# Performance work log

Measured on AMD Instinct MI355X. Metric: run time of the kernel, lower is better.

Reference implementation:

```python
import jax, jax.numpy as jnp
import numpy as np

QD, CD, H, N, Z, R = 1280, 768, 8, 2, 2, 8
BF, S = 16, 4096


def setup_inputs() -> dict:
    key = jax.random.key(0)
    ks = jax.random.split(key, 12)
    inp = {
        "x": jax.random.normal(ks[0], (BF, S, QD), jnp.float32),
        "context": jax.random.normal(ks[1], (BF, N, CD), jnp.float32),
        "Wq": jax.random.normal(ks[2], (QD, QD), jnp.float32) * (1.0 / np.sqrt(QD)),
        "Wk": jax.random.normal(ks[3], (QD, CD), jnp.float32) * (1.0 / np.sqrt(CD)),
        "Ak": jax.random.normal(ks[4], (R, CD), jnp.float32) * 0.01,
        "Bk": jax.random.normal(ks[5], (QD, R), jnp.float32) * 0.01,
        "Wv": jax.random.normal(ks[6], (QD, CD), jnp.float32) * (1.0 / np.sqrt(CD)),
        "Av": jax.random.normal(ks[7], (R, CD), jnp.float32) * 0.01,
        "Bv": jax.random.normal(ks[8], (QD, R), jnp.float32) * 0.01,
        "depth_pe": jax.random.normal(ks[9], (Z, CD), jnp.float32) * 0.02,
        "Wout": jax.random.normal(ks[10], (QD, QD), jnp.float32) * (1.0 / np.sqrt(QD)),
        "bout": jnp.zeros((QD,), jnp.float32),
    }
    return inp


def _lora(t, W, A, B):
    # F.linear(t, W) + F.linear(F.linear(t, A), B)
    return t @ W.T + (t @ A.T) @ B.T


def reference(x, context, Wq, Wk, Ak, Bk, Wv, Av, Bv, depth_pe, Wout, bout):
    bf, s, qd = x.shape
    d = qd // H
    scale = 1.0 / jnp.sqrt(jnp.asarray(d, x.dtype))
    # expand context with depth positional encoding: [bf, N, Z, CD] -> [bf, N*Z, CD]
    ctx3d = (context[:, :, None, :] + depth_pe[None, None, :, :]).reshape(bf, N * Z, -1)
    Q = (x @ Wq.T).reshape(bf, s, H, d).transpose(0, 2, 1, 3)            # bf h s d
    K = _lora(ctx3d, Wk, Ak, Bk).reshape(bf, N * Z, H, d).transpose(0, 2, 1, 3)  # bf h t d
    V = _lora(ctx3d, Wv, Av, Bv).reshape(bf, N * Z, H, d).transpose(0, 2, 1, 3)
    scores = jnp.einsum('bhsd,bhtd->bhst', Q, K) * scale                 # bf h s (n z)
    sigma = jax.nn.sigmoid(scores).reshape(bf, H, s, N, Z)
    sigma_mean = sigma.mean(axis=1)                                      # bf s n z
    opacity = jnp.minimum(sigma_mean.sum(axis=2), 1.0)                   # bf s z
    ones = jnp.ones((bf, s, 1), x.dtype)
    T = jnp.cumprod(jnp.concatenate([ones, 1.0 - opacity], axis=-1), axis=-1)[:, :, :-1]  # bf s z
    weights = (T[:, None, :, None, :] * sigma).reshape(bf, H, s, N * Z)
    out = jnp.einsum('bhst,bhtd->bhsd', weights, V)
    out = out.transpose(0, 2, 1, 3).reshape(bf, s, qd)
    return x + out @ Wout.T + bout
```

## Files before the change

### kernel.cpp

```cpp
#include <hip/hip_runtime.h>

#define QD   1280
#define CD   768
#define NH   8
#define NN   2
#define ZZ   2
#define RR   8
#define BFB  16
#define SS   4096
#define DH   160
#define TT   4
#define OO   32

typedef __attribute__((ext_vector_type(4))) float f32x4;
typedef __attribute__((ext_vector_type(8))) short short8;

__global__ __launch_bounds__(256) void kv_kernel(
    const float* __restrict__ ctx, const float* __restrict__ pe,
    const float* __restrict__ Wk, const float* __restrict__ Ak, const float* __restrict__ Bk,
    const float* __restrict__ Wv, const float* __restrict__ Av, const float* __restrict__ Bv,
    float* __restrict__ Kf, float* __restrict__ Vf)
{
    const int jt = blockIdx.x, t = blockIdx.y, b = blockIdx.z;
    const int n = t >> 1, z = t & 1;
    const int tid = threadIdx.x;
    __shared__ float sctx[CD];
    __shared__ float sa[16];

    for (int c = tid; c < CD; c += 256)
        sctx[c] = ctx[(b * NN + n) * CD + c] + pe[z * CD + c];
    __syncthreads();

    const int wave = tid >> 6, lane = tid & 63;
    for (int q = 0; q < 4; q++) {
        const int idx = wave * 4 + q;
        const float* Arow = (idx < 8 ? Ak : Av) + (idx & 7) * CD;
        float p = 0.f;
        for (int c = lane; c < CD; c += 64) p += sctx[c] * Arow[c];
        for (int off = 32; off; off >>= 1) p += __shfl_down(p, off);
        if (lane == 0) sa[idx] = p;
    }
    __syncthreads();

    const int j = jt * 256 + tid;
    float accK = 0.f, accV = 0.f;
    {
        f32x4 bk0 = *(const f32x4*)(Bk + j * RR);
        f32x4 bk1 = *(const f32x4*)(Bk + j * RR + 4);
        f32x4 bv0 = *(const f32x4*)(Bv + j * RR);
        f32x4 bv1 = *(const f32x4*)(Bv + j * RR + 4);
#pragma unroll
        for (int r = 0; r < 4; r++) {
            accK += sa[r] * bk0[r] + sa[r + 4] * bk1[r];
            accV += sa[8 + r] * bv0[r] + sa[12 + r] * bv1[r];
        }
    }
    const f32x4* wkrow = (const f32x4*)(Wk + j * CD);
    const f32x4* wvrow = (const f32x4*)(Wv + j * CD);
    for (int c4 = 0; c4 < CD / 4; c4++) {
        f32x4 wk = wkrow[c4], wv = wvrow[c4];
#pragma unroll
        for (int u = 0; u < 4; u++) {
            float xc = sctx[c4 * 4 + u];
            accK += xc * wk[u];
            accV += xc * wv[u];
        }
    }
    Kf[(b * TT + t) * QD + j] = accK;
    Vf[(b * TT + t) * QD + j] = accV;
}

__global__ __launch_bounds__(256) void pvw_kernel(
    const float* __restrict__ Wq, const float* __restrict__ Wout,
    const float* __restrict__ Kf, const float* __restrict__ Vf,
    float* __restrict__ P, float* __restrict__ VW)
{
    const int which = blockIdx.x, ht = blockIdx.y, b = blockIdx.z;
    const int h = ht >> 2, t = ht & 3;
    const int tid = threadIdx.x;
    __shared__ float sv[DH];

    if (which == 0) {
        for (int d = tid; d < DH; d += 256) sv[d] = Kf[(b * TT + t) * QD + h * DH + d];
        __syncthreads();
        float acc[5] = {0.f, 0.f, 0.f, 0.f, 0.f};
        for (int d = 0; d < DH; d++) {
            float kd = sv[d];
            const float* wqrow = Wq + (h * DH + d) * QD;
#pragma unroll
            for (int i = 0; i < 5; i++) acc[i] += kd * wqrow[tid + 256 * i];
        }
#pragma unroll
        for (int i = 0; i < 5; i++)
            P[(b * QD + tid + 256 * i) * OO + ht] = acc[i];
    } else {
        for (int d = tid; d < DH; d += 256) sv[d] = Vf[(b * TT + t) * QD + h * DH + d];
        __syncthreads();
        float acc[5] = {0.f, 0.f, 0.f, 0.f, 0.f};
        for (int d4 = 0; d4 < DH / 4; d4++) {
#pragma unroll
            for (int i = 0; i < 5; i++) {
                int j = tid + 256 * i;
                f32x4 w = *(const f32x4*)(Wout + j * QD + h * DH + d4 * 4);
#pragma unroll
                for (int u = 0; u < 4; u++) acc[i] += sv[d4 * 4 + u] * w[u];
            }
        }
#pragma unroll
        for (int i = 0; i < 5; i++)
            VW[(b * OO + ht) * QD + tid + 256 * i] = acc[i];
    }
}

__global__ __launch_bounds__(64) void pfrag_kernel(
    const float* __restrict__ P, unsigned* __restrict__ Pfrag)
{
    const int ksnt = blockIdx.x;
    const int b = blockIdx.y;
    const int ks = ksnt >> 1, nt = ksnt & 1;
    const int l = threadIdx.x;
    const int k0 = ks * 32 + (l >> 4) * 8;
    const int o  = nt * 16 + (l & 15);

    const float* Pb = P + ((size_t)b * QD + k0) * OO + o;
    float v[8];
#pragma unroll
    for (int j = 0; j < 8; j++) v[j] = Pb[j * OO];

    unsigned d[4];
#pragma unroll
    for (int i = 0; i < 4; i++)
        asm("v_cvt_pk_bf16_f32 %0, %1, %2" : "=v"(d[i]) : "v"(v[2 * i]), "v"(v[2 * i + 1]));

    unsigned* dst = Pfrag + ((size_t)(b * 80 + ksnt) * 64 + l) * 4;
    dst[0] = d[0]; dst[1] = d[1]; dst[2] = d[2]; dst[3] = d[3];
}

__global__ __launch_bounds__(256) void scores_kernel(
    const float* __restrict__ x, const unsigned* __restrict__ Pfrag,
    float* __restrict__ Wgt)
{
    const int b = blockIdx.y;
    const int tid = threadIdx.x;
    const int w = tid >> 6, l = tid & 63;
    const int lg = l >> 4, lo16 = l & 15;
    const int rowbase = blockIdx.x * 64 + w * 16;
    const float scale = 0.07905694150420949f;

    f32x4 acc0 = (f32x4){0.f, 0.f, 0.f, 0.f};
    f32x4 acc1 = (f32x4){0.f, 0.f, 0.f, 0.f};

    const float* xr0 = x + ((size_t)b * SS + rowbase + lo16) * QD;
    const unsigned* Pfb = Pfrag + (size_t)b * 80 * 256 + (size_t)l * 4;

    union U { unsigned u[4]; short8 s; };

    for (int ks = 0; ks < 40; ++ks) {
        const int kb = ks * 32 + lg * 8;
        f32x4 x00 = *(const f32x4*)(xr0 + kb);
        f32x4 x01 = *(const f32x4*)(xr0 + kb + 4);
        short8 bf0 = *(const short8*)(Pfb + (size_t)(ks * 2 + 0) * 256);
        short8 bf1 = *(const short8*)(Pfb + (size_t)(ks * 2 + 1) * 256);

        U a0;
        asm("v_cvt_pk_bf16_f32 %0, %1, %2" : "=v"(a0.u[0]) : "v"(x00[0]), "v"(x00[1]));
        asm("v_cvt_pk_bf16_f32 %0, %1, %2" : "=v"(a0.u[1]) : "v"(x00[2]), "v"(x00[3]));
        asm("v_cvt_pk_bf16_f32 %0, %1, %2" : "=v"(a0.u[2]) : "v"(x01[0]), "v"(x01[1]));
        asm("v_cvt_pk_bf16_f32 %0, %1, %2" : "=v"(a0.u[3]) : "v"(x01[2]), "v"(x01[3]));

        acc0 = __builtin_amdgcn_mfma_f32_16x16x32_bf16(a0.s, bf0, acc0, 0, 0, 0);
        acc1 = __builtin_amdgcn_mfma_f32_16x16x32_bf16(a0.s, bf1, acc1, 0, 0, 0);
    }

#pragma unroll
    for (int r = 0; r < 4; ++r) {
        float s0v = 1.f / (1.f + __expf(-acc0[r] * scale));
        float s1v = 1.f / (1.f + __expf(-acc1[r] * scale));
        float contrib = ((l & 1) == 0) ? (s0v + s1v) : 0.f;
        contrib += __shfl_xor(contrib, 1);
        contrib += __shfl_xor(contrib, 2);
        contrib += __shfl_xor(contrib, 4);
        contrib += __shfl_xor(contrib, 8);
        float op0 = fminf(contrib * 0.125f, 1.f);
        float t1 = (l & 1) ? (1.f - op0) : 1.f;
        const int R = rowbase + lg * 4 + r;
        float* Wr = Wgt + ((size_t)b * SS + R) * OO;
        Wr[lo16]      = s0v * t1;
        Wr[lo16 + 16] = s1v * t1;
    }
}

__global__ __launch_bounds__(320) void out_kernel(
    const float* __restrict__ x, const float* __restrict__ bout,
    const float* __restrict__ VW, const float* __restrict__ Wgt,
    float* __restrict__ out)
{
    const int b = blockIdx.y;
    const int s0 = blockIdx.x * 64;
    const int tid = threadIdx.x;

    f32x4 vw[32];
    {
        const float* VWb = VW + (size_t)b * OO * QD + 4 * tid;
#pragma unroll
        for (int ht = 0; ht < 32; ht++) vw[ht] = *(const f32x4*)(VWb + ht * QD);
    }
    f32x4 bo = *(const f32x4*)(bout + 4 * tid);

    const size_t base = ((size_t)b * SS + s0) * QD + 4 * tid;
    const float* wg0 = Wgt + ((size_t)b * SS + s0) * OO;

#pragma unroll 2
    for (int row = 0; row < 64; ++row) {
        f32x4 acc = bo + *(const f32x4*)(x + base + (size_t)row * QD);
        const float* wr = wg0 + row * OO;
#pragma unroll
        for (int ht = 0; ht < 32; ht++) {
            float wv_ = wr[ht];
            acc += wv_ * vw[ht];
        }
        *(f32x4*)(out + base + (size_t)row * QD) = acc;
    }
}

extern "C" void kernel_launch(void* const* d_in, const int* in_sizes, int n_in,
                              void* d_out, int out_size, void* d_ws, size_t ws_size,
                              hipStream_t stream) {
    const float* x    = (const float*)d_in[0];
    const float* ctx  = (const float*)d_in[1];
    const float* Wq   = (const float*)d_in[2];
    const float* Wk   = (const float*)d_in[3];
    const float* Ak   = (const float*)d_in[4];
    const float* Bk   = (const float*)d_in[5];
    const float* Wv   = (const float*)d_in[6];
    const float* Av   = (const float*)d_in[7];
    const float* Bv   = (const float*)d_in[8];
    const float* pe   = (const float*)d_in[9];
    const float* Wout = (const float*)d_in[10];
    const float* bout = (const float*)d_in[11];
    float* out = (float*)d_out;

    float* ws = (float*)d_ws;
    float* Kf = ws;
    float* Vf = ws + 81920;
    float* P  = ws + 163840;
    float* VW = ws + 819200;
    float* Wg = ws + 1474560;
    unsigned* Pfrag = (unsigned*)(ws + 3571712);

    kv_kernel<<<dim3(5, 4, 16), 256, 0, stream>>>(ctx, pe, Wk, Ak, Bk, Wv, Av, Bv, Kf, Vf);
    pvw_kernel<<<dim3(2, 32, 16), 256, 0, stream>>>(Wq, Wout, Kf, Vf, P, VW);
    pfrag_kernel<<<dim3(80, 16), 64, 0, stream>>>(P, Pfrag);
    scores_kernel<<<dim3(64, 16), 256, 0, stream>>>(x, Pfrag, Wg);
    out_kernel<<<dim3(64, 16), 320, 0, stream>>>(x, bout, VW, Wg, out);
}
```

Before: 940.5 us.

## Share weight loads across kv slots in pvw and split-K scores kernel

The pvw kernel now computes all four context slots per head in one block. Each Wq/Wout element is loaded once and reused for four accumulators, where before each slot reloaded the weights, and the grid shrinks to a quarter. The scores kernel doubles to 512 threads and splits the K dimension across two wave groups, combining partial MFMA accumulators through shared memory. This gives more waves to hide memory latency on the x reads, at the cost of a barrier and LDS traffic.

```diff
diff --git a/kernel.cpp b/kernel.cpp
--- a/kernel.cpp
+++ b/kernel.cpp
@@ -75,40 +75,68 @@
     const float* __restrict__ Kf, const float* __restrict__ Vf,
     float* __restrict__ P, float* __restrict__ VW)
 {
-    const int which = blockIdx.x, ht = blockIdx.y, b = blockIdx.z;
-    const int h = ht >> 2, t = ht & 3;
+    const int which = blockIdx.x, h = blockIdx.y, b = blockIdx.z;
     const int tid = threadIdx.x;
-    __shared__ float sv[DH];
+    __shared__ float sv[TT][DH];
+
+    const float* src = (which == 0 ? Kf : Vf);
+    for (int e = tid; e < TT * DH; e += 256) {
+        int t = e / DH, d = e % DH;
+        sv[t][d] = src[(b * TT + t) * QD + h * DH + d];
+    }
+    __syncthreads();
 
     if (which == 0) {
-        for (int d = tid; d < DH; d += 256) sv[d] = Kf[(b * TT + t) * QD + h * DH + d];
-        __syncthreads();
-        float acc[5] = {0.f, 0.f, 0.f, 0.f, 0.f};
+        float acc[5][4];
+#pragma unroll
+        for (int i = 0; i < 5; i++)
+#pragma unroll
+            for (int t = 0; t < 4; t++) acc[i][t] = 0.f;
+
+#pragma unroll 2
         for (int d = 0; d < DH; d++) {
-            float kd = sv[d];
             const float* wqrow = Wq + (h * DH + d) * QD;
-#pragma unroll
-            for (int i = 0; i < 5; i++) acc[i] += kd * wqrow[tid + 256 * i];
-        }
+            float wq[5];
+#pragma unroll
+            for (int i = 0; i < 5; i++) wq[i] = wqrow[tid + 256 * i];
+#pragma unroll
+            for (int i = 0; i < 5; i++)
+#pragma unroll
+                for (int t = 0; t < 4; t++)
+                    acc[i][t] = fmaf(sv[t][d], wq[i], acc[i][t]);
+        }
+#pragma unroll
+        for (int i = 0; i < 5; i++) {
+            int j = tid + 256 * i;
+            f32x4 v = {acc[i][0], acc[i][1], acc[i][2], acc[i][3]};
+            *(f32x4*)(P + ((size_t)(b * QD + j)) * OO + h * 4) = v;
+        }
+    } else {
+        float acc[5][4];
 #pragma unroll
         for (int i = 0; i < 5; i++)
-            P[(b * QD + tid + 256 * i) * OO + ht] = acc[i];
-    } else {
-        for (int d = tid; d < DH; d += 256) sv[d] = Vf[(b * TT + t) * QD + h * DH + d];
-        __syncthreads();
-        float acc[5] = {0.f, 0.f, 0.f, 0.f, 0.f};
+#pragma unroll
+            for (int t = 0; t < 4; t++) acc[i][t] = 0.f;
+
         for (int d4 = 0; d4 < DH / 4; d4++) {
 #pragma unroll
             for (int i = 0; i < 5; i++) {
                 int j = tid + 256 * i;
-                f32x4 w = *(const f32x4*)(Wout + j * QD + h * DH + d4 * 4);
-#pragma unroll
-                for (int u = 0; u < 4; u++) acc[i] += sv[d4 * 4 + u] * w[u];
+                f32x4 w = *(const f32x4*)(Wout + (size_t)j * QD + h * DH + d4 * 4);
+#pragma unroll
+                for (int u = 0; u < 4; u++)
+#pragma unroll
+                    for (int t = 0; t < 4; t++)
+                        acc[i][t] = fmaf(sv[t][d4 * 4 + u], w[u], acc[i][t]);
             }
         }
 #pragma unroll
-        for (int i = 0; i < 5; i++)
-            VW[(b * OO + ht) * QD + tid + 256 * i] = acc[i];
+        for (int i = 0; i < 5; i++) {
+            int j = tid + 256 * i;
+#pragma unroll
+            for (int t = 0; t < 4; t++)
+                VW[((size_t)b * OO + h * 4 + t) * QD + j] = acc[i][t];
+        }
     }
 }
 
@@ -136,26 +164,31 @@
     dst[0] = d[0]; dst[1] = d[1]; dst[2] = d[2]; dst[3] = d[3];
 }
 
-__global__ __launch_bounds__(256) void scores_kernel(
+__global__ __launch_bounds__(512, 8) void scores_kernel(
     const float* __restrict__ x, const unsigned* __restrict__ Pfrag,
     float* __restrict__ Wgt)
 {
     const int b = blockIdx.y;
     const int tid = threadIdx.x;
     const int w = tid >> 6, l = tid & 63;
+    const int g = w & 3;
+    const int khalf = w >> 2;
     const int lg = l >> 4, lo16 = l & 15;
-    const int rowbase = blockIdx.x * 64 + w * 16;
+    const int rowbase = blockIdx.x * 64 + g * 16;
     const float scale = 0.07905694150420949f;
+
+    __shared__ float red[4][64][9];
 
     f32x4 acc0 = (f32x4){0.f, 0.f, 0.f, 0.f};
     f32x4 acc1 = (f32x4){0.f, 0.f, 0.f, 0.f};
 
-    const float* xr0 = x + ((size_t)b * SS + rowbase + lo16) * QD;
-    const unsigned* Pfb = Pfrag + (size_t)b * 80 * 256 + (size_t)l * 4;
+    const float* xr0 = x + ((size_t)b * SS + rowbase + lo16) * QD + khalf * 640;
+    const unsigned* Pfb = Pfrag + (size_t)b * 80 * 256 + (size_t)l * 4
+                        + (size_t)khalf * 40 * 256;
 
     union U { unsigned u[4]; short8 s; };
 
-    for (int ks = 0; ks < 40; ++ks) {
+    for (int ks = 0; ks < 20; ++ks) {
         const int kb = ks * 32 + lg * 8;
         f32x4 x00 = *(const f32x4*)(xr0 + kb);
         f32x4 x01 = *(const f32x4*)(xr0 + kb + 4);
@@ -170,6 +203,22 @@
 
         acc0 = __builtin_amdgcn_mfma_f32_16x16x32_bf16(a0.s, bf0, acc0, 0, 0, 0);
         acc1 = __builtin_amdgcn_mfma_f32_16x16x32_bf16(a0.s, bf1, acc1, 0, 0, 0);
+    }
+
+    if (khalf == 1) {
+#pragma unroll
+        for (int r = 0; r < 4; ++r) {
+            red[g][l][r]     = acc0[r];
+            red[g][l][4 + r] = acc1[r];
+        }
+    }
+    __syncthreads();
+    if (khalf == 1) return;
+
+#pragma unroll
+    for (int r = 0; r < 4; ++r) {
+        acc0[r] += red[g][l][r];
+        acc1[r] += red[g][l][4 + r];
     }
 
 #pragma unroll
@@ -249,8 +298,8 @@
     unsigned* Pfrag = (unsigned*)(ws + 3571712);
 
     kv_kernel<<<dim3(5, 4, 16), 256, 0, stream>>>(ctx, pe, Wk, Ak, Bk, Wv, Av, Bv, Kf, Vf);
-    pvw_kernel<<<dim3(2, 32, 16), 256, 0, stream>>>(Wq, Wout, Kf, Vf, P, VW);
+    pvw_kernel<<<dim3(2, 8, 16), 256, 0, stream>>>(Wq, Wout, Kf, Vf, P, VW);
     pfrag_kernel<<<dim3(80, 16), 64, 0, stream>>>(P, Pfrag);
-    scores_kernel<<<dim3(64, 16), 256, 0, stream>>>(x, Pfrag, Wg);
+    scores_kernel<<<dim3(64, 16), 512, 0, stream>>>(x, Pfrag, Wg);
     out_kernel<<<dim3(64, 16), 320, 0, stream>>>(x, bout, VW, Wg, out);
 }
```

After: 847.7 us. 9.9% less time.
